# Kernel tuning notes

Hardware: AMD Instinct MI355X
Metric: run time of the kernel (lower is better)

Reference implementation:

```python
import jax, jax.numpy as jnp
import numpy as np

B, N, P = 8, 4096, 1024
P4 = P // 4
EPS = 1e-5


def _ln(x, g, b):
    mu = jnp.mean(x, axis=-1, keepdims=True)
    var = jnp.var(x, axis=-1, keepdims=True)
    return (x - mu) * jax.lax.rsqrt(var + EPS) * g + b


def setup_inputs() -> dict:
    key = jax.random.key(0)
    ks = jax.random.split(key, 16)
    s = lambda fan: 1.0 / np.sqrt(fan)
    return {
        "xyz": jax.random.normal(ks[0], (B, N, 3), jnp.float32),
        "x": jax.random.normal(ks[1], (B, N, P), jnp.float32),
        "ln1_g": jnp.ones((P,), jnp.float32),
        "ln1_b": jnp.zeros((P,), jnp.float32),
        "ln2_g": jnp.ones((P,), jnp.float32),
        "ln2_b": jnp.zeros((P,), jnp.float32),
        "qk_w": jax.random.normal(ks[2], (P4, P), jnp.float32) * s(P),   # shared q/k 1x1 conv, no bias
        "v_w": jax.random.normal(ks[3], (P, P), jnp.float32) * s(P),
        "v_b": jax.random.normal(ks[4], (P,), jnp.float32) * s(P),
        "t1_w": jax.random.normal(ks[5], (P, P4), jnp.float32) * s(P4),  # trans_conv
        "t1_b": jax.random.normal(ks[6], (P,), jnp.float32) * s(P4),
        "t2_w": jax.random.normal(ks[7], (P, P4), jnp.float32) * s(P4),  # trans_conv1
        "t2_b": jax.random.normal(ks[8], (P,), jnp.float32) * s(P4),
        "m1_w": jax.random.normal(ks[9], (P, P), jnp.float32) * s(P),
        "m1_b": jax.random.normal(ks[10], (P,), jnp.float32) * s(P),
        "m2_w": jax.random.normal(ks[11], (P, P), jnp.float32) * s(P),
        "m2_b": jax.random.normal(ks[12], (P,), jnp.float32) * s(P),
    }


def reference(xyz, x, ln1_g, ln1_b, ln2_g, ln2_b, qk_w, v_w, v_b,
              t1_w, t1_b, t2_w, t2_b, m1_w, m1_b, m2_w, m2_b):
    # xyz is accepted but unused, matching the torch module. Dropout = eval identity.
    res1 = x
    h = _ln(x, ln1_g, ln1_b)                                   # [B,N,P]
    # TransformerBlock_1 (1x1 convs on h^T [B,P,N] are just matmuls over P)
    x_q = jnp.einsum('op,bnp->bon', qk_w, h)                   # [B,P4,N]
    # k shares weights with q; x_k permuted is x_q transposed
    x_v = jnp.einsum('op,bnp->bno', v_w, h) + v_b              # [B,N,P]
    energy = jnp.einsum('bqn,bkn->bqk', x_q, x_q)              # [B,P4,P4]
    att = jnp.einsum('op,bpk->bok', t1_w, energy) + t1_b[:, None]   # [B,P,P4]
    att = jax.nn.gelu(att, approximate=False)
    att = jnp.einsum('op,bkp->bok', t2_w, att) + t2_b[:, None]      # [B,P,P]
    att = jax.nn.softmax(att, axis=-1)
    t_out = jnp.einsum('bnp,bpq->bnq', x_v, att)               # [B,N,P]
    x1 = t_out + res1
    h2 = _ln(x1, ln2_g, ln2_b)
    m = jax.nn.gelu(h2 @ m1_w.T + m1_b, approximate=False)
    m = m @ m2_w.T + m2_b
    return x1 + m
```

## Files before the change

### kernel.cpp

```cpp
#include <hip/hip_runtime.h>


typedef __attribute__((ext_vector_type(4))) float f32x4;
typedef __attribute__((ext_vector_type(8))) _Float16 h16x8;
typedef __attribute__((ext_vector_type(8))) unsigned short u16x8;
typedef __attribute__((ext_vector_type(4))) unsigned short u16x4;

__device__ __forceinline__ unsigned short f2h(float f) {
  _Float16 h = (_Float16)f;
  return __builtin_bit_cast(unsigned short, h);
}
__device__ __forceinline__ unsigned split16(float f) {
  _Float16 h = (_Float16)f;
  _Float16 l = (_Float16)(f - (float)h);
  return (unsigned)__builtin_bit_cast(unsigned short, h) |
         ((unsigned)__builtin_bit_cast(unsigned short, l) << 16);
}
__device__ __forceinline__ float gelu_f(float x) {
  return 0.5f * x * (1.0f + erff(x * 0.70710678118654752f));
}
__device__ __forceinline__ void gload16(const void* g, void* l) {
  __builtin_amdgcn_global_load_lds(
      (const __attribute__((address_space(1))) unsigned int*)g,
      (__attribute__((address_space(3))) unsigned int*)l, 16, 0, 0);
}

__global__ __launch_bounds__(256)
void ln_kernel(const float* __restrict__ x, const float* __restrict__ g,
               const float* __restrict__ b, unsigned short* __restrict__ hi,
               unsigned short* __restrict__ lo) {
  __shared__ float red[16];
  const size_t base = (size_t)blockIdx.x * 1024;
  const int t = threadIdx.x;
  f32x4 v = *(const f32x4*)&x[base + t * 4];
  float s = v[0] + v[1] + v[2] + v[3];
  float q = v[0] * v[0] + v[1] * v[1] + v[2] * v[2] + v[3] * v[3];
#pragma unroll
  for (int o = 32; o > 0; o >>= 1) { s += __shfl_down(s, o); q += __shfl_down(q, o); }
  const int w = t >> 6;
  if ((t & 63) == 0) { red[w] = s; red[8 + w] = q; }
  __syncthreads();
  s = (red[0] + red[1]) + (red[2] + red[3]);
  q = (red[8] + red[9]) + (red[10] + red[11]);
  const float mu = s * (1.0f / 1024.0f);
  const float var = q * (1.0f / 1024.0f) - mu * mu;
  const float is = rsqrtf(var + 1e-5f);
  f32x4 gg = *(const f32x4*)&g[t * 4];
  f32x4 bb = *(const f32x4*)&b[t * 4];
  u16x4 oh, ol;
#pragma unroll
  for (int j = 0; j < 4; j++) {
    float y = (v[j] - mu) * is * gg[j] + bb[j];
    unsigned p = split16(y);
    oh[j] = (unsigned short)(p & 0xffffu);
    ol[j] = (unsigned short)(p >> 16);
  }
  *(u16x4*)&hi[base + t * 4] = oh;
  if (lo) *(u16x4*)&lo[base + t * 4] = ol;
}

__global__ __launch_bounds__(256)
void cvt_kernel(const float* __restrict__ in, unsigned short* __restrict__ hi,
                unsigned short* __restrict__ lo, int n4) {
  int i = blockIdx.x * 256 + threadIdx.x;
  if (i < n4) {
    f32x4 v = *(const f32x4*)&in[(size_t)i * 4];
    u16x4 oh, ol;
#pragma unroll
    for (int j = 0; j < 4; j++) {
      unsigned p = split16(v[j]);
      oh[j] = (unsigned short)(p & 0xffffu);
      ol[j] = (unsigned short)(p >> 16);
    }
    *(u16x4*)&hi[(size_t)i * 4] = oh;
    if (lo) *(u16x4*)&lo[(size_t)i * 4] = ol;
  }
}

template <int EPI, int SPLIT>
__global__ __launch_bounds__(256)
void gemm16(const unsigned short* __restrict__ Ahi, const unsigned short* __restrict__ Alo,
            const unsigned short* __restrict__ Bhi, const unsigned short* __restrict__ Blo,
            void* __restrict__ Cout, unsigned short* __restrict__ Cout2,
            const float* __restrict__ bias, const float* __restrict__ resIn,
            int K, int lda, int ldb, int ldc,
            long long sA, long long sB, long long sC, long long sRes, int splitK) {
  __shared__ short As[(1 + SPLIT) * 128 * 64];
  __shared__ short Bs[(1 + SPLIT) * 128 * 64];
  const int z = blockIdx.z;
  const int bi = z / splitK, sp = z % splitK;
  const int kLen = K / splitK, kStart = sp * kLen;
  const unsigned short* AH = Ahi + (size_t)bi * sA;
  const unsigned short* BH = Bhi + (size_t)bi * sB;
  const unsigned short* AL = SPLIT ? Alo + (size_t)bi * sA : nullptr;
  const unsigned short* BL = SPLIT ? Blo + (size_t)bi * sB : nullptr;
  const int mBase = blockIdx.y * 128, nBase = blockIdx.x * 128;
  const int t = threadIdx.x, w = t >> 6, l = t & 63;
  const int r16 = l & 15, kq = l >> 4;
  const int wr = (w >> 1) * 64, wc = (w & 1) * 64;
  f32x4 acc[4][4] = {};

  for (int k0 = kStart; k0 < kStart + kLen; k0 += 64) {
#pragma unroll
    for (int it = 0; it < 4; ++it) {
      const int c = it * 256 + t;
      const int row = c >> 3, cc = c & 7;
      const int gc = cc ^ (row & 7);
      const int cbase = it * 256 + w * 64;
      const size_t ga = (size_t)(mBase + row) * lda + k0 + gc * 8;
      const size_t gb = (size_t)(nBase + row) * ldb + k0 + gc * 8;
      gload16(&AH[ga], &As[cbase * 8]);
      gload16(&BH[gb], &Bs[cbase * 8]);
      if constexpr (SPLIT) {
        gload16(&AL[ga], &As[8192 + cbase * 8]);
        gload16(&BL[gb], &Bs[8192 + cbase * 8]);
      }
    }
    asm volatile("s_waitcnt vmcnt(0)" ::: "memory");
    __syncthreads();
#pragma unroll
    for (int kk = 0; kk < 2; ++kk) {
      h16x8 aH[4], bH[4], aL[4], bL[4];
#pragma unroll
      for (int mi = 0; mi < 4; mi++) {
        const int r = wr + mi * 16 + r16;
        const int cc = (kk * 4 + kq) ^ (r & 7);
        aH[mi] = *(const h16x8*)&As[r * 64 + cc * 8];
        if constexpr (SPLIT) aL[mi] = *(const h16x8*)&As[8192 + r * 64 + cc * 8];
      }
#pragma unroll
      for (int ni = 0; ni < 4; ni++) {
        const int r = wc + ni * 16 + r16;
        const int cc = (kk * 4 + kq) ^ (r & 7);
        bH[ni] = *(const h16x8*)&Bs[r * 64 + cc * 8];
        if constexpr (SPLIT) bL[ni] = *(const h16x8*)&Bs[8192 + r * 64 + cc * 8];
      }
#pragma unroll
      for (int mi = 0; mi < 4; mi++)
#pragma unroll
        for (int ni = 0; ni < 4; ni++) {
          acc[mi][ni] = __builtin_amdgcn_mfma_f32_16x16x32_f16(aH[mi], bH[ni], acc[mi][ni], 0, 0, 0);
          if constexpr (SPLIT) {
            acc[mi][ni] = __builtin_amdgcn_mfma_f32_16x16x32_f16(aH[mi], bL[ni], acc[mi][ni], 0, 0, 0);
            acc[mi][ni] = __builtin_amdgcn_mfma_f32_16x16x32_f16(aL[mi], bH[ni], acc[mi][ni], 0, 0, 0);
          }
        }
    }
    __syncthreads();
  }

  unsigned short* C16 = (unsigned short*)Cout + (size_t)z * sC;
  unsigned short* C16b = Cout2 ? Cout2 + (size_t)z * sC : nullptr;
  float* C32 = (float*)Cout + (size_t)z * sC;
  const float* res = (EPI == 2 || EPI == 3) ? (resIn + (size_t)z * sRes) : nullptr;
#pragma unroll
  for (int mi = 0; mi < 4; mi++) {
#pragma unroll
    for (int ni = 0; ni < 4; ni++) {
      const int cl = nBase + wc + ni * 16 + r16;
      float bcol = 0.0f;
      if (EPI == 0 || EPI == 1 || EPI == 3) bcol = bias[cl];
#pragma unroll
      for (int r = 0; r < 4; r++) {
        const int rw = mBase + wr + mi * 16 + kq * 4 + r;
        float v = acc[mi][ni][r] + bcol;
        if (EPI == 6 || EPI == 7) v += bias[rw];
        if (EPI == 1 || EPI == 6) v = gelu_f(v);
        if (EPI == 2 || EPI == 3) v += res[(size_t)rw * ldc + cl];
        const size_t idx = (size_t)rw * ldc + cl;
        if (EPI == 0 || EPI == 1) C16[idx] = f2h(v);
        else if (EPI == 4 || EPI == 6) {
          unsigned p = split16(v);
          C16[idx] = (unsigned short)(p & 0xffffu);
          C16b[idx] = (unsigned short)(p >> 16);
        }
        else C32[idx] = v;
      }
    }
  }
}

__global__ __launch_bounds__(256)
void ereduce_kernel(const float* __restrict__ part, unsigned short* __restrict__ ehi,
                    unsigned short* __restrict__ elo) {
  const size_t idx = (size_t)blockIdx.x * 256 + threadIdx.x;
  const size_t b = idx >> 16, i = idx & 65535;
  const float* p = part + b * (8ull * 65536) + i;
  float s0 = (p[0] + p[65536]) + (p[2 * 65536] + p[3 * 65536]);
  float s1 = (p[4 * 65536] + p[5 * 65536]) + (p[6 * 65536] + p[7 * 65536]);
  unsigned pk = split16(s0 + s1);
  ehi[idx] = (unsigned short)(pk & 0xffffu);
  elo[idx] = (unsigned short)(pk >> 16);
}

__global__ __launch_bounds__(256)
void smax_t_kernel(const float* __restrict__ a2, unsigned short* __restrict__ attT) {
  __shared__ float S[8][1028];
  __shared__ float inv[8];
  const int t = threadIdx.x;
  const int b = blockIdx.y;
  const int o0 = blockIdx.x * 8;
  const float* src = a2 + ((size_t)b * 1024 + o0) * 1024;
#pragma unroll
  for (int i = 0; i < 8; i++)
    *(f32x4*)&S[i][t * 4] = *(const f32x4*)&src[(size_t)i * 1024 + t * 4];
  __syncthreads();
  const int w = t >> 6, l = t & 63;
  for (int rr = 0; rr < 2; rr++) {
    const int r = w * 2 + rr;
    float m = -1e30f;
#pragma unroll
    for (int i = 0; i < 16; i++) m = fmaxf(m, S[r][l + i * 64]);
#pragma unroll
    for (int o = 32; o > 0; o >>= 1) m = fmaxf(m, __shfl_xor(m, o));
    float ssum = 0.0f;
#pragma unroll
    for (int i = 0; i < 16; i++) {
      float e = expf(S[r][l + i * 64] - m);
      S[r][l + i * 64] = e;
      ssum += e;
    }
#pragma unroll
    for (int o = 32; o > 0; o >>= 1) ssum += __shfl_xor(ssum, o);
    if (l == 0) inv[r] = 1.0f / ssum;
  }
  __syncthreads();
  float iv[8];
#pragma unroll
  for (int r = 0; r < 8; r++) iv[r] = inv[r];
#pragma unroll
  for (int i = 0; i < 4; i++) {
    const int k = i * 256 + t;
    u16x8 ov;
#pragma unroll
    for (int r = 0; r < 8; r++) ov[r] = f2h(S[r][k] * iv[r]);
    *(u16x8*)&attT[((size_t)b * 1024 + k) * 1024 + o0] = ov;
  }
}

extern "C" void kernel_launch(void* const* d_in, const int* in_sizes, int n_in,
                              void* d_out, int out_size, void* d_ws, size_t ws_size,
                              hipStream_t stream) {
  (void)in_sizes; (void)n_in; (void)out_size; (void)ws_size;
  const float* x     = (const float*)d_in[1];
  const float* ln1_g = (const float*)d_in[2];
  const float* ln1_b = (const float*)d_in[3];
  const float* ln2_g = (const float*)d_in[4];
  const float* ln2_b = (const float*)d_in[5];
  const float* qk_w  = (const float*)d_in[6];
  const float* v_w   = (const float*)d_in[7];
  const float* v_b   = (const float*)d_in[8];
  const float* t1_w  = (const float*)d_in[9];
  const float* t1_b  = (const float*)d_in[10];
  const float* t2_w  = (const float*)d_in[11];
  const float* t2_b  = (const float*)d_in[12];
  const float* m1_w  = (const float*)d_in[13];
  const float* m1_b  = (const float*)d_in[14];
  const float* m2_w  = (const float*)d_in[15];
  const float* m2_b  = (const float*)d_in[16];

  char* ws = (char*)d_ws;
  unsigned short* hhi  = (unsigned short*)(ws + 0);
  unsigned short* hlo  = (unsigned short*)(ws + 67108864);
  unsigned short* Qthi = (unsigned short*)(ws + 134217728);
  unsigned short* Qtlo = (unsigned short*)(ws + 150994944);
  float*          part = (float*)(ws + 167772160);
  unsigned short* Ehi  = (unsigned short*)(ws + 184549376);
  unsigned short* Elo  = (unsigned short*)(ws + 185597952);
  unsigned short* Ghi  = (unsigned short*)(ws + 186646528);
  unsigned short* Glo  = (unsigned short*)(ws + 190840832);
  float*          a2   = (float*)(ws + 195035136);
  unsigned short* attT = (unsigned short*)(ws + 228589568);
  unsigned short* xv   = (unsigned short*)(ws + 245366784);
  float*          x1   = (float*)(ws + 312475648);
  unsigned short* wqh  = (unsigned short*)(ws + 446693376);
  unsigned short* wql  = (unsigned short*)(ws + 447217664);
  unsigned short* wv   = (unsigned short*)(ws + 447741952);
  unsigned short* wt1h = (unsigned short*)(ws + 449839104);
  unsigned short* wt1l = (unsigned short*)(ws + 450363392);
  unsigned short* wt2h = (unsigned short*)(ws + 450887680);
  unsigned short* wt2l = (unsigned short*)(ws + 451411968);
  unsigned short* wm1  = (unsigned short*)(ws + 451936256);
  unsigned short* wm2  = (unsigned short*)(ws + 454033408);
  unsigned short* h2 = hhi;
  unsigned short* gb = hlo;
  float* out = (float*)d_out;

  cvt_kernel<<<dim3(256),  dim3(256), 0, stream>>>(qk_w, wqh, wql, 65536);
  cvt_kernel<<<dim3(1024), dim3(256), 0, stream>>>(v_w, wv, nullptr, 262144);
  cvt_kernel<<<dim3(256),  dim3(256), 0, stream>>>(t1_w, wt1h, wt1l, 65536);
  cvt_kernel<<<dim3(256),  dim3(256), 0, stream>>>(t2_w, wt2h, wt2l, 65536);
  cvt_kernel<<<dim3(1024), dim3(256), 0, stream>>>(m1_w, wm1, nullptr, 262144);
  cvt_kernel<<<dim3(1024), dim3(256), 0, stream>>>(m2_w, wm2, nullptr, 262144);
  ln_kernel<<<dim3(32768), dim3(256), 0, stream>>>(x, ln1_g, ln1_b, hhi, hlo);
  gemm16<4, 1><<<dim3(32, 2, 8), dim3(256), 0, stream>>>(
      wqh, wql, hhi, hlo, Qthi, Qtlo, nullptr, nullptr,
      1024, 1024, 1024, 4096, 0, 4194304, 1048576, 0, 1);
  gemm16<0, 0><<<dim3(8, 256, 1), dim3(256), 0, stream>>>(
      hhi, nullptr, wv, nullptr, xv, nullptr, v_b, nullptr,
      1024, 1024, 1024, 1024, 0, 0, 0, 0, 1);
  gemm16<5, 1><<<dim3(2, 2, 64), dim3(256), 0, stream>>>(
      Qthi, Qtlo, Qthi, Qtlo, part, nullptr, nullptr, nullptr,
      4096, 4096, 4096, 256, 1048576, 1048576, 65536, 0, 8);
  ereduce_kernel<<<dim3(2048), dim3(256), 0, stream>>>(part, Ehi, Elo);
  gemm16<6, 1><<<dim3(2, 8, 8), dim3(256), 0, stream>>>(
      wt1h, wt1l, Ehi, Elo, Ghi, Glo, t1_b, nullptr,
      256, 256, 256, 256, 0, 65536, 262144, 0, 1);
  gemm16<7, 1><<<dim3(8, 8, 8), dim3(256), 0, stream>>>(
      wt2h, wt2l, Ghi, Glo, a2, nullptr, t2_b, nullptr,
      256, 256, 256, 1024, 0, 262144, 1048576, 0, 1);
  smax_t_kernel<<<dim3(128, 8), dim3(256), 0, stream>>>(a2, attT);
  gemm16<2, 0><<<dim3(8, 32, 8), dim3(256), 0, stream>>>(
      xv, nullptr, attT, nullptr, x1, nullptr, nullptr, x,
      1024, 1024, 1024, 1024, 4194304, 1048576, 4194304, 4194304, 1);
  ln_kernel<<<dim3(32768), dim3(256), 0, stream>>>(x1, ln2_g, ln2_b, h2, nullptr);
  gemm16<1, 0><<<dim3(8, 256, 1), dim3(256), 0, stream>>>(
      h2, nullptr, wm1, nullptr, gb, nullptr, m1_b, nullptr,
      1024, 1024, 1024, 1024, 0, 0, 0, 0, 1);
  gemm16<3, 0><<<dim3(8, 256, 1), dim3(256), 0, stream>>>(
      gb, nullptr, wm2, nullptr, out, nullptr, m2_b, x1,
      1024, 1024, 1024, 1024, 0, 0, 0, 0, 1);
}
```

Before: 757.8 us.

## Double-buffer LDS tiles in non-split GEMM and remap workgroups across XCDs

For the non-split fp16 GEMM path, the shared-memory tiles are double-buffered: the next K tile is loaded with global_load_lds while MFMAs run on the current one, removing the load-then-compute serialization. The split path keeps its original single-buffered loop. Workgroup indices are also remapped into chunks so that neighbouring tiles land on the same XCD, improving L2 reuse. Non-split kernels now allocate the larger 2x LDS footprint, which may lower occupancy.

Measured after the change: 733.5 us. 3.2% less time.

```diff
diff --git a/kernel.cpp b/kernel.cpp
--- a/kernel.cpp
+++ b/kernel.cpp
@@ -85,8 +85,8 @@
             const float* __restrict__ bias, const float* __restrict__ resIn,
             int K, int lda, int ldb, int ldc,
             long long sA, long long sB, long long sC, long long sRes, int splitK) {
-  __shared__ short As[(1 + SPLIT) * 128 * 64];
-  __shared__ short Bs[(1 + SPLIT) * 128 * 64];
+  __shared__ short As[16384];
+  __shared__ short Bs[16384];
   const int z = blockIdx.z;
   const int bi = z / splitK, sp = z % splitK;
   const int kLen = K / splitK, kStart = sp * kLen;
@@ -94,59 +94,114 @@
   const unsigned short* BH = Bhi + (size_t)bi * sB;
   const unsigned short* AL = SPLIT ? Alo + (size_t)bi * sA : nullptr;
   const unsigned short* BL = SPLIT ? Blo + (size_t)bi * sB : nullptr;
-  const int mBase = blockIdx.y * 128, nBase = blockIdx.x * 128;
+
+  int bx = blockIdx.x, by = blockIdx.y;
+  {
+    const int nwg = gridDim.x * gridDim.y;
+    if ((nwg & 7) == 0 && nwg >= 16) {
+      const int flat = bx + gridDim.x * by;
+      const int chunk = nwg >> 3;
+      const int nf = (flat & 7) * chunk + (flat >> 3);
+      bx = nf % gridDim.x;
+      by = nf / gridDim.x;
+    }
+  }
+  const int mBase = by * 128, nBase = bx * 128;
   const int t = threadIdx.x, w = t >> 6, l = t & 63;
   const int r16 = l & 15, kq = l >> 4;
   const int wr = (w >> 1) * 64, wc = (w & 1) * 64;
   f32x4 acc[4][4] = {};
 
-  for (int k0 = kStart; k0 < kStart + kLen; k0 += 64) {
+  auto stage_hi = [&](int buf, int k0) {
 #pragma unroll
     for (int it = 0; it < 4; ++it) {
       const int c = it * 256 + t;
       const int row = c >> 3, cc = c & 7;
       const int gc = cc ^ (row & 7);
       const int cbase = it * 256 + w * 64;
-      const size_t ga = (size_t)(mBase + row) * lda + k0 + gc * 8;
-      const size_t gb = (size_t)(nBase + row) * ldb + k0 + gc * 8;
-      gload16(&AH[ga], &As[cbase * 8]);
-      gload16(&BH[gb], &Bs[cbase * 8]);
-      if constexpr (SPLIT) {
+      gload16(&AH[(size_t)(mBase + row) * lda + k0 + gc * 8], &As[buf * 8192 + cbase * 8]);
+      gload16(&BH[(size_t)(nBase + row) * ldb + k0 + gc * 8], &Bs[buf * 8192 + cbase * 8]);
+    }
+  };
+
+  if constexpr (!SPLIT) {
+    const int nt = kLen >> 6;
+    stage_hi(0, kStart);
+    asm volatile("s_waitcnt vmcnt(0)" ::: "memory");
+    __syncthreads();
+    int cur = 0;
+    for (int ts = 0; ts < nt; ++ts) {
+      if (ts + 1 < nt) stage_hi(cur ^ 1, kStart + (ts + 1) * 64);
+#pragma unroll
+      for (int kk = 0; kk < 2; ++kk) {
+        h16x8 aH[4], bH[4];
+#pragma unroll
+        for (int mi = 0; mi < 4; mi++) {
+          const int r = wr + mi * 16 + r16;
+          const int cc = (kk * 4 + kq) ^ (r & 7);
+          aH[mi] = *(const h16x8*)&As[cur * 8192 + r * 64 + cc * 8];
+        }
+#pragma unroll
+        for (int ni = 0; ni < 4; ni++) {
+          const int r = wc + ni * 16 + r16;
+          const int cc = (kk * 4 + kq) ^ (r & 7);
+          bH[ni] = *(const h16x8*)&Bs[cur * 8192 + r * 64 + cc * 8];
+        }
+#pragma unroll
+        for (int mi = 0; mi < 4; mi++)
+#pragma unroll
+          for (int ni = 0; ni < 4; ni++)
+            acc[mi][ni] = __builtin_amdgcn_mfma_f32_16x16x32_f16(aH[mi], bH[ni], acc[mi][ni], 0, 0, 0);
+      }
+      asm volatile("s_waitcnt vmcnt(0)" ::: "memory");
+      __syncthreads();
+      cur ^= 1;
+    }
+  } else {
+    for (int k0 = kStart; k0 < kStart + kLen; k0 += 64) {
+#pragma unroll
+      for (int it = 0; it < 4; ++it) {
+        const int c = it * 256 + t;
+        const int row = c >> 3, cc = c & 7;
+        const int gc = cc ^ (row & 7);
+        const int cbase = it * 256 + w * 64;
+        const size_t ga = (size_t)(mBase + row) * lda + k0 + gc * 8;
+        const size_t gb = (size_t)(nBase + row) * ldb + k0 + gc * 8;
+        gload16(&AH[ga], &As[cbase * 8]);
+        gload16(&BH[gb], &Bs[cbase * 8]);
         gload16(&AL[ga], &As[8192 + cbase * 8]);
         gload16(&BL[gb], &Bs[8192 + cbase * 8]);
       }
-    }
-    asm volatile("s_waitcnt vmcnt(0)" ::: "memory");
-    __syncthreads();
-#pragma unroll
-    for (int kk = 0; kk < 2; ++kk) {
-      h16x8 aH[4], bH[4], aL[4], bL[4];
-#pragma unroll
-      for (int mi = 0; mi < 4; mi++) {
-        const int r = wr + mi * 16 + r16;
-        const int cc = (kk * 4 + kq) ^ (r & 7);
-        aH[mi] = *(const h16x8*)&As[r * 64 + cc * 8];
-        if constexpr (SPLIT) aL[mi] = *(const h16x8*)&As[8192 + r * 64 + cc * 8];
-      }
-#pragma unroll
-      for (int ni = 0; ni < 4; ni++) {
-        const int r = wc + ni * 16 + r16;
-        const int cc = (kk * 4 + kq) ^ (r & 7);
-        bH[ni] = *(const h16x8*)&Bs[r * 64 + cc * 8];
-        if constexpr (SPLIT) bL[ni] = *(const h16x8*)&Bs[8192 + r * 64 + cc * 8];
-      }
-#pragma unroll
-      for (int mi = 0; mi < 4; mi++)
+      asm volatile("s_waitcnt vmcnt(0)" ::: "memory");
+      __syncthreads();
+#pragma unroll
+      for (int kk = 0; kk < 2; ++kk) {
+        h16x8 aH[4], bH[4], aL[4], bL[4];
+#pragma unroll
+        for (int mi = 0; mi < 4; mi++) {
+          const int r = wr + mi * 16 + r16;
+          const int cc = (kk * 4 + kq) ^ (r & 7);
+          aH[mi] = *(const h16x8*)&As[r * 64 + cc * 8];
+          aL[mi] = *(const h16x8*)&As[8192 + r * 64 + cc * 8];
+        }
 #pragma unroll
         for (int ni = 0; ni < 4; ni++) {
-          acc[mi][ni] = __builtin_amdgcn_mfma_f32_16x16x32_f16(aH[mi], bH[ni], acc[mi][ni], 0, 0, 0);
-          if constexpr (SPLIT) {
+          const int r = wc + ni * 16 + r16;
+          const int cc = (kk * 4 + kq) ^ (r & 7);
+          bH[ni] = *(const h16x8*)&Bs[r * 64 + cc * 8];
+          bL[ni] = *(const h16x8*)&Bs[8192 + r * 64 + cc * 8];
+        }
+#pragma unroll
+        for (int mi = 0; mi < 4; mi++)
+#pragma unroll
+          for (int ni = 0; ni < 4; ni++) {
+            acc[mi][ni] = __builtin_amdgcn_mfma_f32_16x16x32_f16(aH[mi], bH[ni], acc[mi][ni], 0, 0, 0);
             acc[mi][ni] = __builtin_amdgcn_mfma_f32_16x16x32_f16(aH[mi], bL[ni], acc[mi][ni], 0, 0, 0);
             acc[mi][ni] = __builtin_amdgcn_mfma_f32_16x16x32_f16(aL[mi], bH[ni], acc[mi][ni], 0, 0, 0);
           }
-        }
-    }
-    __syncthreads();
+      }
+      __syncthreads();
+    }
   }
 
   unsigned short* C16 = (unsigned short*)Cout + (size_t)z * sC;
```
